# Performance work log

Measured on AMD Instinct MI355X. Metric: run time of the kernel, lower is better.

Reference implementation:

```python
import jax, jax.numpy as jnp
import numpy as np

EC = 256   # ec
CT = 512   # ct
NH = 8     # heads
K = 3      # adaptive pool output
HC = EC // NH
CH = (256, 512, 1024)
HW = (48, 24, 12)
BS = 32
NT = 512   # number of text queries


def _ln(x, g, b, eps=1e-5):
    m = jnp.mean(x, axis=-1, keepdims=True)
    v = jnp.mean((x - m) ** 2, axis=-1, keepdims=True)
    return (x - m) * jax.lax.rsqrt(v + eps) * g + b


def _adaptive_max_pool(x, k):
    # H, W divisible by k -> uniform bins, identical to AdaptiveMaxPool2d
    B, C, H, W = x.shape
    return x.reshape(B, C, k, H // k, k, W // k).max(axis=(3, 5))


def setup_inputs() -> dict:
    key = jax.random.key(0)
    ks = jax.random.split(key, 32)
    d = {}
    for i, (c, s) in enumerate(zip(CH, HW)):
        d[f"x{i}"] = jax.random.normal(ks[i], (BS, c, s, s), jnp.float32)
    d["text"] = jax.random.normal(ks[3], (BS, NT, CT), jnp.float32)
    # 1x1 conv projections (stored as [C_in, EC] matrices)
    for i, c in enumerate(CH):
        d[f"w{i}"] = jax.random.normal(ks[4 + i], (c, EC), jnp.float32) / np.sqrt(c).astype(np.float32)
        d[f"cb{i}"] = jax.random.normal(ks[7 + i], (EC,), jnp.float32) * 0.02
    # LayerNorm + Linear for query (ct->ec), key/value (ec->ec)
    d["q_ln_g"] = jnp.ones((CT,), jnp.float32); d["q_ln_b"] = jnp.zeros((CT,), jnp.float32)
    d["k_ln_g"] = jnp.ones((EC,), jnp.float32); d["k_ln_b"] = jnp.zeros((EC,), jnp.float32)
    d["v_ln_g"] = jnp.ones((EC,), jnp.float32); d["v_ln_b"] = jnp.zeros((EC,), jnp.float32)
    d["q_w"] = jax.random.normal(ks[10], (CT, EC), jnp.float32) / np.sqrt(CT).astype(np.float32)
    d["q_b"] = jax.random.normal(ks[11], (EC,), jnp.float32) * 0.02
    d["k_w"] = jax.random.normal(ks[12], (EC, EC), jnp.float32) / np.sqrt(EC).astype(np.float32)
    d["k_b"] = jax.random.normal(ks[13], (EC,), jnp.float32) * 0.02
    d["v_w"] = jax.random.normal(ks[14], (EC, EC), jnp.float32) / np.sqrt(EC).astype(np.float32)
    d["v_b"] = jax.random.normal(ks[15], (EC,), jnp.float32) * 0.02
    d["proj_w"] = jax.random.normal(ks[16], (EC, CT), jnp.float32) / np.sqrt(EC).astype(np.float32)
    d["proj_b"] = jax.random.normal(ks[17], (CT,), jnp.float32) * 0.02
    return d


def reference(x0, x1, x2, text, w0, cb0, w1, cb1, w2, cb2,
              q_ln_g, q_ln_b, k_ln_g, k_ln_b, v_ln_g, v_ln_b,
              q_w, q_b, k_w, k_b, v_w, v_b, proj_w, proj_b):
    bs = x0.shape[0]
    feats = []
    for x, w, b in ((x0, w0, cb0), (x1, w1, cb1), (x2, w2, cb2)):
        p = jnp.einsum('bchw,ce->behw', x, w) + b[None, :, None, None]  # 1x1 conv
        feats.append(_adaptive_max_pool(p, K).reshape(bs, EC, K * K))
    xc = jnp.concatenate(feats, axis=-1).transpose(0, 2, 1)  # (bs, 27, ec)

    q = _ln(text, q_ln_g, q_ln_b) @ q_w + q_b   # (bs, NT, ec)
    k = _ln(xc, k_ln_g, k_ln_b) @ k_w + k_b     # (bs, 27, ec)
    v = _ln(xc, v_ln_g, v_ln_b) @ v_w + v_b     # (bs, 27, ec)

    q = q.reshape(bs, -1, NH, HC)
    k = k.reshape(bs, -1, NH, HC)
    v = v.reshape(bs, -1, NH, HC)

    aw = jnp.einsum('bnmc,bkmc->bmnk', q, k) / np.sqrt(HC).astype(np.float32)
    aw = jax.nn.softmax(aw, axis=-1)
    o = jnp.einsum('bmnk,bkmc->bnmc', aw, v).reshape(bs, -1, EC)
    return o @ proj_w + proj_b + text  # scale=False -> scale == 1.0
```

## Files before the change

kernel.cpp:

```cpp
#include <hip/hip_runtime.h>
#include <stdint.h>

#define DEVFN __device__ __forceinline__

using f32x4   = __attribute__((ext_vector_type(4)))  float;
using f32x8   = __attribute__((ext_vector_type(8)))  float;
using f32x16  = __attribute__((ext_vector_type(16))) float;
using us4     = __attribute__((ext_vector_type(4)))  unsigned short;
using us8     = __attribute__((ext_vector_type(8)))  unsigned short;
using u32x4   = __attribute__((ext_vector_type(4)))  unsigned int;
using bf16x8  = __attribute__((ext_vector_type(8)))  __bf16;

DEVFN unsigned short f2b(float x){
    union { float f; unsigned u; } v; v.f = x;
    unsigned r = v.u + 0x7FFFu + ((v.u >> 16) & 1u);
    return (unsigned short)(r >> 16);
}
DEVFN float b2f(unsigned short u){
    union { unsigned u; float f; } v; v.u = ((unsigned)u) << 16; return v.f;
}
DEVFN bf16x8 ld_bf16x8(const unsigned short* p){
    return __builtin_bit_cast(bf16x8, *(const us8*)p);
}
DEVFN bf16x8 pack_bf16x8v(f32x8 f){
    us8 u;
#pragma unroll
    for (int j = 0; j < 8; ++j) u[j] = f2b(f[j]);
    return __builtin_bit_cast(bf16x8, u);
}
DEVFN f32x16 zero16(){
    f32x16 z;
#pragma unroll
    for (int i = 0; i < 16; ++i) z[i] = 0.f;
    return z;
}
DEVFN f32x16 mfma_bf16(bf16x8 a, bf16x8 b, f32x16 c){
    return __builtin_amdgcn_mfma_f32_32x32x16_bf16(a, b, c, 0, 0, 0);
}
DEVFN void gload_lds16(const unsigned short* g, unsigned short* l){
    __builtin_amdgcn_global_load_lds(
        (const __attribute__((address_space(1))) unsigned int*)(const void*)g,
        (__attribute__((address_space(3))) unsigned int*)(void*)l,
        16, 0, 0);
}
template<int HW>
DEVFN f32x8 loadA8(const float* ap){
    f32x8 v;
#pragma unroll
    for (int j = 0; j < 8; ++j) v[j] = ap[(size_t)j * HW];
    return v;
}

__global__ __launch_bounds__(256) void k_prep(
        const float* __restrict__ w0, const float* __restrict__ w1,
        const float* __restrict__ w2, const float* __restrict__ qw,
        const float* __restrict__ pw, const float* __restrict__ kw,
        const float* __restrict__ vw,
        unsigned short* __restrict__ o0, unsigned short* __restrict__ o1,
        unsigned short* __restrict__ o2, unsigned short* __restrict__ oq,
        unsigned short* __restrict__ op, unsigned short* __restrict__ ok,
        unsigned short* __restrict__ ov){
    int gid = blockIdx.x * 256 + threadIdx.x;
    const float* in; unsigned short* out; int t, E;
    if (gid < 8192)       { in = w0; out = o0; t = gid;         E = 256; }
    else if (gid < 24576) { in = w1; out = o1; t = gid - 8192;  E = 256; }
    else if (gid < 57344) { in = w2; out = o2; t = gid - 24576; E = 256; }
    else if (gid < 73728) { in = qw; out = oq; t = gid - 57344; E = 256; }
    else if (gid < 90112) { in = pw; out = op; t = gid - 73728; E = 512; }
    else if (gid < 98304) { in = kw; out = ok; t = gid - 90112; E = 256; }
    else                  { in = vw; out = ov; t = gid - 98304; E = 256; }
    int lane = t & 63, fn = t >> 6;
    int nt, ks;
    if (E == 512){ nt = fn & 15; ks = fn >> 4; }
    else         { nt = fn & 7;  ks = fn >> 3; }
    int c0 = ks*16 + (lane >> 5)*8, e = nt*32 + (lane & 31);
    us8 u;
#pragma unroll
    for (int j = 0; j < 8; ++j) u[j] = f2b(in[(size_t)(c0 + j) * E + e]);
    *(us8*)(out + (size_t)t * 8) = u;
}

DEVFN void comp2(f32x16 (&acc)[4], f32x8 a, const unsigned short* bsmr, int kk, int ntb, int lane){
    bf16x8 A = pack_bf16x8v(a);
#pragma unroll
    for (int i = 0; i < 4; ++i){
        bf16x8 B = ld_bf16x8(bsmr + (kk*8 + ntb + i) * 512 + lane * 8);
        acc[i] = mfma_bf16(A, B, acc[i]);
    }
}

template<int C, int WIMG, int BINW>
DEVFN void conv_sub(const float* __restrict__ X, const unsigned short* __restrict__ WF,
                    unsigned short* bsm0, unsigned short* bsm1,
                    int b, int bin, int sub, int ntb, float* rmax){
    const int HW = WIMG * WIMG;
    const int NCH = C / 32;
    int w8 = threadIdx.x >> 6, lane = threadIdx.x & 63, lo = lane & 31, hi = lane >> 5;
    int binr = bin / 3, binc = bin % 3;
    int prow, pcol;
    if constexpr (BINW == 16){ prow = sub*2 + (lo>>4); pcol = lo & 15; }
    else if constexpr (BINW == 8){ prow = sub*4 + (lo>>3); pcol = lo & 7; }
    else { prow = (lo & 15) >> 2; pcol = lo & 3; }
    int gr = binr * BINW + prow, gc = binc * BINW + pcol;
    const float* Xk = X + (size_t)b * C * HW + gr * WIMG + gc + (size_t)hi * 8 * HW;

    f32x16 acc[4];
#pragma unroll
    for (int i = 0; i < 4; ++i) acc[i] = zero16();

    auto stage = [&](unsigned short* dst, int ch){
        const unsigned short* src = WF + (size_t)ch * 8192 + w8 * 1024 + lane * 8;
        unsigned short* dl = dst + w8 * 1024;
        gload_lds16(src,       dl);
        gload_lds16(src + 512, dl + 512);
    };

    __syncthreads();
    stage(bsm0, 0);
    f32x8 a0 = loadA8<HW>(Xk);
    f32x8 a1 = loadA8<HW>(Xk + (size_t)16 * HW);
    __syncthreads();

    unsigned short* cur = bsm0;
    unsigned short* nxt = bsm1;
    for (int c = 0; c < NCH; ++c){
        f32x8 p0, p1;
        bool more = (c + 1 < NCH);
        if (more){
            stage(nxt, c + 1);
            const float* Xn = Xk + (size_t)(c + 1) * 32 * HW;
            p0 = loadA8<HW>(Xn);
            p1 = loadA8<HW>(Xn + (size_t)16 * HW);
        }
        comp2(acc, a0, cur, 0, ntb, lane);
        comp2(acc, a1, cur, 1, ntb, lane);
        __syncthreads();
        if (more){ a0 = p0; a1 = p1; }
        unsigned short* t = cur; cur = nxt; nxt = t;
    }
#pragma unroll
    for (int i = 0; i < 4; ++i){
        float m = acc[i][0];
#pragma unroll
        for (int r = 1; r < 16; ++r) m = fmaxf(m, acc[i][r]);
        rmax[i] = fmaxf(rmax[i], m);
    }
}

__global__ __launch_bounds__(512, 2) void k_conv_pool(
        const float* __restrict__ x0, const float* __restrict__ x1, const float* __restrict__ x2,
        const unsigned short* __restrict__ wt0, const unsigned short* __restrict__ wt1,
        const unsigned short* __restrict__ wt2,
        const float* __restrict__ cb0, const float* __restrict__ cb1, const float* __restrict__ cb2,
        float* __restrict__ xc){
    __shared__ __attribute__((aligned(16))) unsigned short bsm0[8192];
    __shared__ __attribute__((aligned(16))) unsigned short bsm1[8192];
    __shared__ float red[8][4][32];
    int blk = blockIdx.x, w = threadIdx.x >> 6, lane = threadIdx.x & 63;
    int lo = lane & 31, hi = lane >> 5;
    int ntb = (w >> 2) * 4;
    float rmax[4];
#pragma unroll
    for (int i = 0; i < 4; ++i) rmax[i] = -3.4e38f;

    if (blk < 96){
        int b = blk / 3, q = blk % 3;
        int bin = q*4 + (w & 3);
        int bc = bin <= 8 ? bin : 8;
        conv_sub<1024, 12, 4>(x2, wt2, bsm0, bsm1, b, bc, 0, ntb, rmax);
#pragma unroll
        for (int i = 0; i < 4; ++i){
            float m = fmaxf(rmax[i], __shfl_xor(rmax[i], 32));
            if (hi == 0 && bin <= 8){
                int e = (ntb + i)*32 + lo;
                xc[((size_t)b*27 + 18 + bin)*256 + e] = m + cb2[e];
            }
        }
    } else if (blk < 256){
        int r = blk - 96, b = r / 5, p = r % 5;
        int binA = 2*p;
        bool hasB = (2*p + 1 <= 8);
        int binB = hasB ? 2*p + 1 : binA;
        int bin = ((w >> 1) & 1) ? binB : binA;
        conv_sub<512, 24, 8>(x1, wt1, bsm0, bsm1, b, bin, w & 1, ntb, rmax);
#pragma unroll
        for (int i = 0; i < 4; ++i){
            float m = fmaxf(rmax[i], __shfl_xor(rmax[i], 32));
            if (hi == 0) red[w][i][lo] = m;
        }
        __syncthreads();
        int t = threadIdx.x;
        int binIdx = t >> 8, e = t & 255;
        int half = e >> 7, ntl = (e >> 5) & 3, l = e & 31;
        int w0 = half*4 + binIdx*2;
        float m = fmaxf(red[w0][ntl][l], red[w0+1][ntl][l]);
        if (binIdx == 0)      xc[((size_t)b*27 + 9 + binA)*256 + e] = m + cb1[e];
        else if (hasB)        xc[((size_t)b*27 + 9 + binB)*256 + e] = m + cb1[e];
    } else {
        int r = blk - 256, b = r / 9, bin = r % 9;
        int s0i = w & 3;
        conv_sub<256, 48, 16>(x0, wt0, bsm0, bsm1, b, bin, s0i,     ntb, rmax);
        conv_sub<256, 48, 16>(x0, wt0, bsm0, bsm1, b, bin, s0i + 4, ntb, rmax);
#pragma unroll
        for (int i = 0; i < 4; ++i){
            float m = fmaxf(rmax[i], __shfl_xor(rmax[i], 32));
            if (hi == 0) red[w][i][lo] = m;
        }
        __syncthreads();
        int t = threadIdx.x;
        if (t < 256){
            int e = t, half = e >> 7, ntl = (e >> 5) & 3, l = e & 31;
            int wb = half * 4;
            float m = fmaxf(fmaxf(red[wb][ntl][l], red[wb+1][ntl][l]),
                            fmaxf(red[wb+2][ntl][l], red[wb+3][ntl][l]));
            xc[((size_t)b*27 + bin)*256 + e] = m + cb0[e];
        }
    }
}

__global__ __launch_bounds__(128) void k_lnq(const float* __restrict__ text,
        const float* __restrict__ g, const float* __restrict__ bb,
        const unsigned short* __restrict__ qwt, const float* __restrict__ qb,
        unsigned short* __restrict__ qout){
    __shared__ unsigned short alds[32][520];
    int w = threadIdx.x >> 6, lane = threadIdx.x & 63, lo = lane & 31, hi = lane >> 5;
    size_t row0 = (size_t)blockIdx.x * 32;

    const float* gp = g  + lane * 8;
    const float* bp = bb + lane * 8;
    f32x4 g0 = *(const f32x4*)gp, g1 = *(const f32x4*)(gp+4);
    f32x4 b0 = *(const f32x4*)bp, b1 = *(const f32x4*)(bp+4);
#pragma unroll
    for (int it = 0; it < 16; ++it){
        int r = it * 2 + w;
        const float* p = text + (row0 + r) * 512 + lane * 8;
        f32x4 a = *(const f32x4*)p;
        f32x4 c = *(const f32x4*)(p + 4);
        float s = a[0]+a[1]+a[2]+a[3]+c[0]+c[1]+c[2]+c[3];
#pragma unroll
        for (int off = 32; off; off >>= 1) s += __shfl_xor(s, off);
        float mean = s * (1.f/512.f);
        float d[8];
        d[0]=a[0]-mean; d[1]=a[1]-mean; d[2]=a[2]-mean; d[3]=a[3]-mean;
        d[4]=c[0]-mean; d[5]=c[1]-mean; d[6]=c[2]-mean; d[7]=c[3]-mean;
        float vs = d[0]*d[0]+d[1]*d[1]+d[2]*d[2]+d[3]*d[3]+d[4]*d[4]+d[5]*d[5]+d[6]*d[6]+d[7]*d[7];
#pragma unroll
        for (int off = 32; off; off >>= 1) vs += __shfl_xor(vs, off);
        float rstd = rsqrtf(vs * (1.f/512.f) + 1e-5f);
        us8 o;
#pragma unroll
        for (int j = 0; j < 4; ++j) o[j]   = f2b(d[j]  *rstd*g0[j] + b0[j]);
#pragma unroll
        for (int j = 0; j < 4; ++j) o[4+j] = f2b(d[4+j]*rstd*g1[j] + b1[j]);
        *(us8*)(&alds[r][lane * 8]) = o;
    }
    __syncthreads();

    f32x16 acc[4];
#pragma unroll
    for (int i = 0; i < 4; ++i) acc[i] = zero16();
    const unsigned short* wf = qwt + (size_t)lane * 8;
    for (int ks = 0; ks < 32; ++ks){
        bf16x8 a = ld_bf16x8(&alds[lo][ks*16 + hi*8]);
#pragma unroll
        for (int i = 0; i < 4; ++i){
            int nt = w*4 + i;
            bf16x8 bfr = ld_bf16x8(wf + (size_t)(ks*8 + nt) * 512);
            acc[i] = mfma_bf16(a, bfr, acc[i]);
        }
    }
#pragma unroll
    for (int i = 0; i < 4; ++i){
        int e = (w*4 + i) * 32 + lo;
        float qbias = qb[e];
#pragma unroll
        for (int r = 0; r < 16; ++r){
            size_t row = row0 + (r & 3) + 8 * (r >> 2) + 4 * hi;
            qout[row * 256 + e] = f2b(acc[i][r] + qbias);
        }
    }
}

__global__ __launch_bounds__(256) void k_kv(const float* __restrict__ xc,
        const float* __restrict__ kg, const float* __restrict__ kb,
        const float* __restrict__ vg, const float* __restrict__ vb,
        const unsigned short* __restrict__ kwt, const unsigned short* __restrict__ vwt,
        const float* __restrict__ k_bias, const float* __restrict__ v_bias,
        float* __restrict__ kout, float* __restrict__ vout){
    __shared__ unsigned short lnk[32][264];
    __shared__ unsigned short lnv[32][264];
    int w = threadIdx.x >> 6, lane = threadIdx.x & 63, lo = lane & 31, hi = lane >> 5;
    size_t row0 = (size_t)blockIdx.x * 32;
    int c0 = lane * 4;
    f32x4 kgv = *(const f32x4*)(kg + c0), kbv = *(const f32x4*)(kb + c0);
    f32x4 vgv = *(const f32x4*)(vg + c0), vbv = *(const f32x4*)(vb + c0);
#pragma unroll
    for (int rr = 0; rr < 8; ++rr){
        int r = w * 8 + rr;
        f32x4 xv = *(const f32x4*)(xc + (row0 + r) * 256 + c0);
        float s = xv[0]+xv[1]+xv[2]+xv[3];
#pragma unroll
        for (int off = 32; off; off >>= 1) s += __shfl_xor(s, off);
        float mean = s * (1.f/256.f);
        float d0 = xv[0]-mean, d1 = xv[1]-mean, d2 = xv[2]-mean, d3 = xv[3]-mean;
        float vs = d0*d0 + d1*d1 + d2*d2 + d3*d3;
#pragma unroll
        for (int off = 32; off; off >>= 1) vs += __shfl_xor(vs, off);
        float rstd = rsqrtf(vs * (1.f/256.f) + 1e-5f);
        us4 uk, uv;
        uk[0] = f2b(d0*rstd*kgv[0] + kbv[0]); uv[0] = f2b(d0*rstd*vgv[0] + vbv[0]);
        uk[1] = f2b(d1*rstd*kgv[1] + kbv[1]); uv[1] = f2b(d1*rstd*vgv[1] + vbv[1]);
        uk[2] = f2b(d2*rstd*kgv[2] + kbv[2]); uv[2] = f2b(d2*rstd*vgv[2] + vbv[2]);
        uk[3] = f2b(d3*rstd*kgv[3] + kbv[3]); uv[3] = f2b(d3*rstd*vgv[3] + vbv[3]);
        *(us4*)(&lnk[r][c0]) = uk;
        *(us4*)(&lnv[r][c0]) = uv;
    }
    __syncthreads();

    f32x16 acc[4];
#pragma unroll
    for (int i = 0; i < 4; ++i) acc[i] = zero16();
    const unsigned short* lds = (w < 2) ? &lnk[0][0] : &lnv[0][0];
    const unsigned short* wf  = ((w < 2) ? kwt : vwt) + (size_t)lane * 8;
    int ntb = (w & 1) * 4;
    for (int ks = 0; ks < 16; ++ks){
        bf16x8 a = ld_bf16x8(lds + lo*264 + ks*16 + hi*8);
#pragma unroll
        for (int i = 0; i < 4; ++i){
            int nt = ntb + i;
            bf16x8 bfr = ld_bf16x8(wf + (size_t)(ks*8 + nt) * 512);
            acc[i] = mfma_bf16(a, bfr, acc[i]);
        }
    }
    const float* bias = (w < 2) ? k_bias : v_bias;
    float* outp = (w < 2) ? kout : vout;
#pragma unroll
    for (int i = 0; i < 4; ++i){
        int e = (ntb + i) * 32 + lo;
        float bv = bias[e];
#pragma unroll
        for (int r = 0; r < 16; ++r){
            size_t row = row0 + (r & 3) + 8 * (r >> 2) + 4 * hi;
            outp[row * 256 + e] = acc[i][r] + bv;
        }
    }
}

__global__ __launch_bounds__(256, 3) void k_attnproj(const unsigned short* __restrict__ qbf,
        const float* __restrict__ kbuf, const float* __restrict__ vbuf,
        const unsigned short* __restrict__ pwt, const float* __restrict__ pb,
        const float* __restrict__ text, float* __restrict__ out){
    int b = blockIdx.x >> 4;
    int rg = blockIdx.x & 15;
    __shared__ unsigned short klds[32][264];
    __shared__ unsigned short vT[256][36];
    __shared__ unsigned short qolds[32][264];
    int tid = threadIdx.x;
    int w = tid >> 6, lane = tid & 63, lo = lane & 31, hi = lane >> 5;
    size_t grow0 = (size_t)b * 512 + rg * 32;

    for (int i = tid; i < 27 * 64; i += 256){
        int row = i >> 6, c4 = (i & 63) << 2;
        f32x4 kv = *(const f32x4*)(kbuf + ((size_t)b*27 + row) * 256 + c4);
        us4 u; u[0]=f2b(kv[0]); u[1]=f2b(kv[1]); u[2]=f2b(kv[2]); u[3]=f2b(kv[3]);
        *(us4*)(&klds[row][c4]) = u;
    }
    for (int i = tid; i < 330; i += 256){
        int row = 27 + i / 66, c4 = (i % 66) * 4;
        us4 z = {0,0,0,0};
        *(us4*)(&klds[row][c4]) = z;
    }
    {
        int ch = tid;
        for (int k = 0; k < 27; ++k)
            vT[ch][k] = f2b(vbuf[((size_t)b*27 + k) * 256 + ch]);
#pragma unroll
        for (int k = 27; k < 36; ++k) vT[ch][k] = 0;
    }
    for (int i = tid; i < 1024; i += 256){
        int row = i >> 5, c8 = (i & 31) << 3;
        *(us8*)(&qolds[row][c8]) = *(const us8*)(qbf + (grow0 + row) * 256 + c8);
    }
    __syncthreads();

#pragma unroll
    for (int hh = 0; hh < 2; ++hh){
        int h = w + hh * 4;
        int hc = h * 32;
        f32x16 s = zero16();
        {
            bf16x8 A0 = ld_bf16x8(&klds[lo][hc + hi*8]);
            bf16x8 B0 = ld_bf16x8(&qolds[lo][hc + hi*8]);
            s = mfma_bf16(A0, B0, s);
            bf16x8 A1 = ld_bf16x8(&klds[lo][hc + 16 + hi*8]);
            bf16x8 B1 = ld_bf16x8(&qolds[lo][hc + 16 + hi*8]);
            s = mfma_bf16(A1, B1, s);
        }
        float mx = -3.4e38f;
#pragma unroll
        for (int r = 0; r < 16; ++r){
            bool valid = hi ? (r < 12) : (r != 15);
            if (valid) mx = fmaxf(mx, s[r]);
        }
        mx = fmaxf(mx, __shfl_xor(mx, 32));
        float p[16]; float sum = 0.f;
#pragma unroll
        for (int r = 0; r < 16; ++r){
            bool valid = hi ? (r < 12) : (r != 15);
            p[r] = valid ? __expf((s[r] - mx) * 0.17677669529663687f) : 0.f;
            sum += p[r];
        }
        sum += __shfl_xor(sum, 32);
        float inv = 1.f / sum;
        unsigned pd[8];
#pragma unroll
        for (int i = 0; i < 8; ++i)
            pd[i] = (unsigned)f2b(p[2*i]*inv) | ((unsigned)f2b(p[2*i+1]*inv) << 16);

        f32x16 o = zero16();
#pragma unroll
        for (int c = 0; c < 2; ++c){
            unsigned own0 = hi ? pd[4*c+2] : pd[4*c];
            unsigned own1 = hi ? pd[4*c+3] : pd[4*c+1];
            unsigned snd0 = hi ? pd[4*c]   : pd[4*c+2];
            unsigned snd1 = hi ? pd[4*c+1] : pd[4*c+3];
            unsigned rcv0 = (unsigned)__shfl_xor((int)snd0, 32);
            unsigned rcv1 = (unsigned)__shfl_xor((int)snd1, 32);
            u32x4 bd;
            bd[0] = hi ? rcv0 : own0;
            bd[1] = hi ? rcv1 : own1;
            bd[2] = hi ? own0 : rcv0;
            bd[3] = hi ? own1 : rcv1;
            bf16x8 B = __builtin_bit_cast(bf16x8, bd);
            bf16x8 A = ld_bf16x8(&vT[hc + lo][c*16 + hi*8]);
            o = mfma_bf16(A, B, o);
        }
#pragma unroll
        for (int g = 0; g < 4; ++g){
            us4 u;
#pragma unroll
            for (int j = 0; j < 4; ++j) u[j] = f2b(o[g*4 + j]);
            *(us4*)(&qolds[lo][hc + g*8 + hi*4]) = u;
        }
    }
    __syncthreads();

    f32x16 acc[4];
#pragma unroll
    for (int i = 0; i < 4; ++i) acc[i] = zero16();
    const unsigned short* wf = pwt + (size_t)lane * 8;
    for (int ks = 0; ks < 16; ++ks){
        bf16x8 a = ld_bf16x8(&qolds[lo][ks*16 + hi*8]);
#pragma unroll
        for (int i = 0; i < 4; ++i){
            int nt = w*4 + i;
            bf16x8 bfr = ld_bf16x8(wf + (size_t)(ks*16 + nt) * 512);
            acc[i] = mfma_bf16(a, bfr, acc[i]);
        }
    }
#pragma unroll
    for (int i = 0; i < 4; ++i){
        int ct = (w*4 + i) * 32 + lo;
        float pbias = pb[ct];
#pragma unroll
        for (int r = 0; r < 16; ++r){
            size_t row = grow0 + (r & 3) + 8 * (r >> 2) + 4 * hi;
            out[row * 512 + ct] = acc[i][r] + pbias + text[row * 512 + ct];
        }
    }
}

extern "C" void kernel_launch(void* const* d_in, const int* in_sizes, int n_in,
                              void* d_out, int out_size, void* d_ws, size_t ws_size,
                              hipStream_t stream) {
    (void)in_sizes; (void)n_in; (void)out_size; (void)ws_size;
    const float* x0     = (const float*)d_in[0];
    const float* x1     = (const float*)d_in[1];
    const float* x2     = (const float*)d_in[2];
    const float* text   = (const float*)d_in[3];
    const float* w0     = (const float*)d_in[4];
    const float* cb0    = (const float*)d_in[5];
    const float* w1     = (const float*)d_in[6];
    const float* cb1    = (const float*)d_in[7];
    const float* w2     = (const float*)d_in[8];
    const float* cb2    = (const float*)d_in[9];
    const float* q_ln_g = (const float*)d_in[10];
    const float* q_ln_b = (const float*)d_in[11];
    const float* k_ln_g = (const float*)d_in[12];
    const float* k_ln_b = (const float*)d_in[13];
    const float* v_ln_g = (const float*)d_in[14];
    const float* v_ln_b = (const float*)d_in[15];
    const float* q_w    = (const float*)d_in[16];
    const float* q_b    = (const float*)d_in[17];
    const float* k_w    = (const float*)d_in[18];
    const float* k_b    = (const float*)d_in[19];
    const float* v_w    = (const float*)d_in[20];
    const float* v_b    = (const float*)d_in[21];
    const float* proj_w = (const float*)d_in[22];
    const float* proj_b = (const float*)d_in[23];
    float* out = (float*)d_out;

    char* wsb = (char*)d_ws; size_t off = 0;
    auto take = [&](size_t bytes) -> void* {
        void* p = wsb + off; off += (bytes + 255) & ~(size_t)255; return p;
    };
    unsigned short* qbf    = (unsigned short*)take((size_t)16384 * 256 * 2);
    float*          xc     = (float*)take((size_t)32 * 27 * 256 * 4);
    float*          kbuf   = (float*)take((size_t)32 * 27 * 256 * 4);
    float*          vbuf   = (float*)take((size_t)32 * 27 * 256 * 4);
    unsigned short* wt0    = (unsigned short*)take((size_t)256 * 256 * 2);
    unsigned short* wt1    = (unsigned short*)take((size_t)256 * 512 * 2);
    unsigned short* wt2    = (unsigned short*)take((size_t)256 * 1024 * 2);
    unsigned short* qwt    = (unsigned short*)take((size_t)256 * 512 * 2);
    unsigned short* pwt    = (unsigned short*)take((size_t)512 * 256 * 2);
    unsigned short* kwt    = (unsigned short*)take((size_t)256 * 256 * 2);
    unsigned short* vwt    = (unsigned short*)take((size_t)256 * 256 * 2);

    k_prep<<<416, 256, 0, stream>>>(w0, w1, w2, q_w, proj_w, k_w, v_w,
                                    wt0, wt1, wt2, qwt, pwt, kwt, vwt);
    k_conv_pool<<<544, 512, 0, stream>>>(x0, x1, x2, wt0, wt1, wt2, cb0, cb1, cb2, xc);
    k_lnq<<<512, 128, 0, stream>>>(text, q_ln_g, q_ln_b, qwt, q_b, qbf);
    k_kv<<<27, 256, 0, stream>>>(xc, k_ln_g, k_ln_b, v_ln_g, v_ln_b,
                                 kwt, vwt, k_b, v_b, kbuf, vbuf);
    k_attnproj<<<512, 256, 0, stream>>>(qbf, kbuf, vbuf, pwt, proj_b, text, out);
}
```

Baseline: 138.9 us.

## Merge conv-pool and text LayerNorm+Q-projection into one heterogeneous launch

Combines the conv/pool kernel and the text LayerNorm + Q projection kernel into a single grid of 1056 blocks. Blocks below 544 run the conv path and the rest run the LN+Q path, with 8 waves each computing one 32-column tile. This removes one kernel launch boundary and lets the two independent stages share the GPU concurrently. In exchange, the LN+Q blocks now use 512 threads and the shared-memory footprint and register pressure set by the conv path, which may lower occupancy for them.

```diff
diff --git a/kernel.cpp b/kernel.cpp
--- a/kernel.cpp
+++ b/kernel.cpp
@@ -147,136 +147,128 @@
     }
 }
 
-__global__ __launch_bounds__(512, 2) void k_conv_pool(
+__global__ __launch_bounds__(512, 2) void k_convlnq(
         const float* __restrict__ x0, const float* __restrict__ x1, const float* __restrict__ x2,
         const unsigned short* __restrict__ wt0, const unsigned short* __restrict__ wt1,
         const unsigned short* __restrict__ wt2,
         const float* __restrict__ cb0, const float* __restrict__ cb1, const float* __restrict__ cb2,
-        float* __restrict__ xc){
-    __shared__ __attribute__((aligned(16))) unsigned short bsm0[8192];
-    __shared__ __attribute__((aligned(16))) unsigned short bsm1[8192];
-    __shared__ float red[8][4][32];
+        float* __restrict__ xc,
+        const float* __restrict__ text, const float* __restrict__ qg,
+        const float* __restrict__ qbb, const unsigned short* __restrict__ qwt,
+        const float* __restrict__ qb, unsigned short* __restrict__ qout){
+    __shared__ __attribute__((aligned(16))) char smem[36864];
+    unsigned short* bsm0 = (unsigned short*)smem;
+    unsigned short* bsm1 = (unsigned short*)(smem + 16384);
+    float (*red)[4][32] = (float (*)[4][32])(smem + 32768);
     int blk = blockIdx.x, w = threadIdx.x >> 6, lane = threadIdx.x & 63;
     int lo = lane & 31, hi = lane >> 5;
-    int ntb = (w >> 2) * 4;
-    float rmax[4];
-#pragma unroll
-    for (int i = 0; i < 4; ++i) rmax[i] = -3.4e38f;
-
-    if (blk < 96){
-        int b = blk / 3, q = blk % 3;
-        int bin = q*4 + (w & 3);
-        int bc = bin <= 8 ? bin : 8;
-        conv_sub<1024, 12, 4>(x2, wt2, bsm0, bsm1, b, bc, 0, ntb, rmax);
-#pragma unroll
-        for (int i = 0; i < 4; ++i){
-            float m = fmaxf(rmax[i], __shfl_xor(rmax[i], 32));
-            if (hi == 0 && bin <= 8){
-                int e = (ntb + i)*32 + lo;
-                xc[((size_t)b*27 + 18 + bin)*256 + e] = m + cb2[e];
+
+    if (blk < 544){
+        int ntb = (w >> 2) * 4;
+        float rmax[4];
+#pragma unroll
+        for (int i = 0; i < 4; ++i) rmax[i] = -3.4e38f;
+
+        if (blk < 96){
+            int b = blk / 3, q = blk % 3;
+            int bin = q*4 + (w & 3);
+            int bc = bin <= 8 ? bin : 8;
+            conv_sub<1024, 12, 4>(x2, wt2, bsm0, bsm1, b, bc, 0, ntb, rmax);
+#pragma unroll
+            for (int i = 0; i < 4; ++i){
+                float m = fmaxf(rmax[i], __shfl_xor(rmax[i], 32));
+                if (hi == 0 && bin <= 8){
+                    int e = (ntb + i)*32 + lo;
+                    xc[((size_t)b*27 + 18 + bin)*256 + e] = m + cb2[e];
+                }
             }
-        }
-    } else if (blk < 256){
-        int r = blk - 96, b = r / 5, p = r % 5;
-        int binA = 2*p;
-        bool hasB = (2*p + 1 <= 8);
-        int binB = hasB ? 2*p + 1 : binA;
-        int bin = ((w >> 1) & 1) ? binB : binA;
-        conv_sub<512, 24, 8>(x1, wt1, bsm0, bsm1, b, bin, w & 1, ntb, rmax);
-#pragma unroll
-        for (int i = 0; i < 4; ++i){
-            float m = fmaxf(rmax[i], __shfl_xor(rmax[i], 32));
-            if (hi == 0) red[w][i][lo] = m;
+        } else if (blk < 256){
+            int r = blk - 96, b = r / 5, p = r % 5;
+            int binA = 2*p;
+            bool hasB = (2*p + 1 <= 8);
+            int binB = hasB ? 2*p + 1 : binA;
+            int bin = ((w >> 1) & 1) ? binB : binA;
+            conv_sub<512, 24, 8>(x1, wt1, bsm0, bsm1, b, bin, w & 1, ntb, rmax);
+#pragma unroll
+            for (int i = 0; i < 4; ++i){
+                float m = fmaxf(rmax[i], __shfl_xor(rmax[i], 32));
+                if (hi == 0) red[w][i][lo] = m;
+            }
+            __syncthreads();
+            int t = threadIdx.x;
+            int binIdx = t >> 8, e = t & 255;
+            int half = e >> 7, ntl = (e >> 5) & 3, l = e & 31;
+            int w0 = half*4 + binIdx*2;
+            float m = fmaxf(red[w0][ntl][l], red[w0+1][ntl][l]);
+            if (binIdx == 0)      xc[((size_t)b*27 + 9 + binA)*256 + e] = m + cb1[e];
+            else if (hasB)        xc[((size_t)b*27 + 9 + binB)*256 + e] = m + cb1[e];
+        } else {
+            int r = blk - 256, b = r / 9, bin = r % 9;
+            int s0i = w & 3;
+            conv_sub<256, 48, 16>(x0, wt0, bsm0, bsm1, b, bin, s0i,     ntb, rmax);
+            conv_sub<256, 48, 16>(x0, wt0, bsm0, bsm1, b, bin, s0i + 4, ntb, rmax);
+#pragma unroll
+            for (int i = 0; i < 4; ++i){
+                float m = fmaxf(rmax[i], __shfl_xor(rmax[i], 32));
+                if (hi == 0) red[w][i][lo] = m;
+            }
+            __syncthreads();
+            int t = threadIdx.x;
+            if (t < 256){
+                int e = t, half = e >> 7, ntl = (e >> 5) & 3, l = e & 31;
+                int wb = half * 4;
+                float m = fmaxf(fmaxf(red[wb][ntl][l], red[wb+1][ntl][l]),
+                                fmaxf(red[wb+2][ntl][l], red[wb+3][ntl][l]));
+                xc[((size_t)b*27 + bin)*256 + e] = m + cb0[e];
+            }
+        }
+    } else {
+        unsigned short* alds = (unsigned short*)smem;
+        size_t row0 = (size_t)(blk - 544) * 32;
+        const float* gp = qg  + lane * 8;
+        const float* bp = qbb + lane * 8;
+        f32x4 g0 = *(const f32x4*)gp, g1 = *(const f32x4*)(gp+4);
+        f32x4 b0 = *(const f32x4*)bp, b1 = *(const f32x4*)(bp+4);
+#pragma unroll
+        for (int it = 0; it < 4; ++it){
+            int r = it * 8 + w;
+            const float* p = text + (row0 + r) * 512 + lane * 8;
+            f32x4 a = *(const f32x4*)p;
+            f32x4 c = *(const f32x4*)(p + 4);
+            float s = a[0]+a[1]+a[2]+a[3]+c[0]+c[1]+c[2]+c[3];
+#pragma unroll
+            for (int off = 32; off; off >>= 1) s += __shfl_xor(s, off);
+            float mean = s * (1.f/512.f);
+            float d[8];
+            d[0]=a[0]-mean; d[1]=a[1]-mean; d[2]=a[2]-mean; d[3]=a[3]-mean;
+            d[4]=c[0]-mean; d[5]=c[1]-mean; d[6]=c[2]-mean; d[7]=c[3]-mean;
+            float vs = d[0]*d[0]+d[1]*d[1]+d[2]*d[2]+d[3]*d[3]+d[4]*d[4]+d[5]*d[5]+d[6]*d[6]+d[7]*d[7];
+#pragma unroll
+            for (int off = 32; off; off >>= 1) vs += __shfl_xor(vs, off);
+            float rstd = rsqrtf(vs * (1.f/512.f) + 1e-5f);
+            us8 o;
+#pragma unroll
+            for (int j = 0; j < 4; ++j) o[j]   = f2b(d[j]  *rstd*g0[j] + b0[j]);
+#pragma unroll
+            for (int j = 0; j < 4; ++j) o[4+j] = f2b(d[4+j]*rstd*g1[j] + b1[j]);
+            *(us8*)(alds + (size_t)r * 520 + lane * 8) = o;
         }
         __syncthreads();
-        int t = threadIdx.x;
-        int binIdx = t >> 8, e = t & 255;
-        int half = e >> 7, ntl = (e >> 5) & 3, l = e & 31;
-        int w0 = half*4 + binIdx*2;
-        float m = fmaxf(red[w0][ntl][l], red[w0+1][ntl][l]);
-        if (binIdx == 0)      xc[((size_t)b*27 + 9 + binA)*256 + e] = m + cb1[e];
-        else if (hasB)        xc[((size_t)b*27 + 9 + binB)*256 + e] = m + cb1[e];
-    } else {
-        int r = blk - 256, b = r / 9, bin = r % 9;
-        int s0i = w & 3;
-        conv_sub<256, 48, 16>(x0, wt0, bsm0, bsm1, b, bin, s0i,     ntb, rmax);
-        conv_sub<256, 48, 16>(x0, wt0, bsm0, bsm1, b, bin, s0i + 4, ntb, rmax);
-#pragma unroll
-        for (int i = 0; i < 4; ++i){
-            float m = fmaxf(rmax[i], __shfl_xor(rmax[i], 32));
-            if (hi == 0) red[w][i][lo] = m;
-        }
-        __syncthreads();
-        int t = threadIdx.x;
-        if (t < 256){
-            int e = t, half = e >> 7, ntl = (e >> 5) & 3, l = e & 31;
-            int wb = half * 4;
-            float m = fmaxf(fmaxf(red[wb][ntl][l], red[wb+1][ntl][l]),
-                            fmaxf(red[wb+2][ntl][l], red[wb+3][ntl][l]));
-            xc[((size_t)b*27 + bin)*256 + e] = m + cb0[e];
-        }
-    }
-}
-
-__global__ __launch_bounds__(128) void k_lnq(const float* __restrict__ text,
-        const float* __restrict__ g, const float* __restrict__ bb,
-        const unsigned short* __restrict__ qwt, const float* __restrict__ qb,
-        unsigned short* __restrict__ qout){
-    __shared__ unsigned short alds[32][520];
-    int w = threadIdx.x >> 6, lane = threadIdx.x & 63, lo = lane & 31, hi = lane >> 5;
-    size_t row0 = (size_t)blockIdx.x * 32;
-
-    const float* gp = g  + lane * 8;
-    const float* bp = bb + lane * 8;
-    f32x4 g0 = *(const f32x4*)gp, g1 = *(const f32x4*)(gp+4);
-    f32x4 b0 = *(const f32x4*)bp, b1 = *(const f32x4*)(bp+4);
-#pragma unroll
-    for (int it = 0; it < 16; ++it){
-        int r = it * 2 + w;
-        const float* p = text + (row0 + r) * 512 + lane * 8;
-        f32x4 a = *(const f32x4*)p;
-        f32x4 c = *(const f32x4*)(p + 4);
-        float s = a[0]+a[1]+a[2]+a[3]+c[0]+c[1]+c[2]+c[3];
-#pragma unroll
-        for (int off = 32; off; off >>= 1) s += __shfl_xor(s, off);
-        float mean = s * (1.f/512.f);
-        float d[8];
-        d[0]=a[0]-mean; d[1]=a[1]-mean; d[2]=a[2]-mean; d[3]=a[3]-mean;
-        d[4]=c[0]-mean; d[5]=c[1]-mean; d[6]=c[2]-mean; d[7]=c[3]-mean;
-        float vs = d[0]*d[0]+d[1]*d[1]+d[2]*d[2]+d[3]*d[3]+d[4]*d[4]+d[5]*d[5]+d[6]*d[6]+d[7]*d[7];
-#pragma unroll
-        for (int off = 32; off; off >>= 1) vs += __shfl_xor(vs, off);
-        float rstd = rsqrtf(vs * (1.f/512.f) + 1e-5f);
-        us8 o;
-#pragma unroll
-        for (int j = 0; j < 4; ++j) o[j]   = f2b(d[j]  *rstd*g0[j] + b0[j]);
-#pragma unroll
-        for (int j = 0; j < 4; ++j) o[4+j] = f2b(d[4+j]*rstd*g1[j] + b1[j]);
-        *(us8*)(&alds[r][lane * 8]) = o;
-    }
-    __syncthreads();
-
-    f32x16 acc[4];
-#pragma unroll
-    for (int i = 0; i < 4; ++i) acc[i] = zero16();
-    const unsigned short* wf = qwt + (size_t)lane * 8;
-    for (int ks = 0; ks < 32; ++ks){
-        bf16x8 a = ld_bf16x8(&alds[lo][ks*16 + hi*8]);
-#pragma unroll
-        for (int i = 0; i < 4; ++i){
-            int nt = w*4 + i;
+
+        f32x16 acc = zero16();
+        const unsigned short* wf = qwt + (size_t)lane * 8;
+        int nt = w;
+        for (int ks = 0; ks < 32; ++ks){
+            bf16x8 a = ld_bf16x8(alds + (size_t)lo * 520 + ks*16 + hi*8);
             bf16x8 bfr = ld_bf16x8(wf + (size_t)(ks*8 + nt) * 512);
-            acc[i] = mfma_bf16(a, bfr, acc[i]);
-        }
-    }
-#pragma unroll
-    for (int i = 0; i < 4; ++i){
-        int e = (w*4 + i) * 32 + lo;
+            acc = mfma_bf16(a, bfr, acc);
+        }
+        int e = nt * 32 + lo;
         float qbias = qb[e];
 #pragma unroll
         for (int r = 0; r < 16; ++r){
             size_t row = row0 + (r & 3) + 8 * (r >> 2) + 4 * hi;
-            qout[row * 256 + e] = f2b(acc[i][r] + qbias);
+            qout[row * 256 + e] = f2b(acc[r] + qbias);
         }
     }
 }
@@ -518,8 +510,8 @@
 
     k_prep<<<416, 256, 0, stream>>>(w0, w1, w2, q_w, proj_w, k_w, v_w,
                                     wt0, wt1, wt2, qwt, pwt, kwt, vwt);
-    k_conv_pool<<<544, 512, 0, stream>>>(x0, x1, x2, wt0, wt1, wt2, cb0, cb1, cb2, xc);
-    k_lnq<<<512, 128, 0, stream>>>(text, q_ln_g, q_ln_b, qwt, q_b, qbf);
+    k_convlnq<<<1056, 512, 0, stream>>>(x0, x1, x2, wt0, wt1, wt2, cb0, cb1, cb2, xc,
+                                        text, q_ln_g, q_ln_b, qwt, q_b, qbf);
     k_kv<<<27, 256, 0, stream>>>(xc, k_ln_g, k_ln_b, v_ln_g, v_ln_b,
                                  kwt, vwt, k_b, v_b, kbuf, vbuf);
     k_attnproj<<<512, 256, 0, stream>>>(qbf, kbuf, vbuf, pwt, proj_b, text, out);
```

Result: faster. 120.9 us, median of 2 (-13.0%).
